# Optimization experiments

Hardware: AMD Instinct MI355X
Metric: run time of the kernel (lower is better)

The kernel has to match this reference:

```python
import jax, jax.numpy as jnp
import numpy as np

WS = 6          # window size
NUM_HEADS = 6
HEAD_DIM = 32   # dim=192 / 6 heads
SCALE = HEAD_DIM ** -0.5


def _rel_pos_index(ws):
    # Faithful to the torch buffer construction (torch.meshgrid default 'ij').
    coords = np.stack(np.meshgrid(np.arange(ws), np.arange(ws), np.arange(ws), indexing='ij'))  # [3,ws,ws,ws]
    flat = coords.reshape(3, -1)                       # [3, ws^3]
    rel = flat[:, :, None] - flat[:, None, :]          # [3, N, N]
    rel = rel.transpose(1, 2, 0).astype(np.int64)      # [N, N, 3]
    rel += ws - 1
    rel[..., 0] *= 3 * ws - 1
    rel[..., 1] *= 2 * ws - 1
    return rel.sum(-1)                                 # [N, N]

REL_INDEX = jnp.asarray(_rel_pos_index(WS))            # [216, 216] int


def setup_inputs() -> dict:
    key = jax.random.key(0)
    k1, k2, k3, k4 = jax.random.split(key, 4)
    B, N, C = 1024, WS ** 3, NUM_HEADS * HEAD_DIM
    return {
        "x": jax.random.normal(k1, (B, N, C), dtype=jnp.float32),
        "qkv_w": jax.random.normal(k2, (3 * C, C), dtype=jnp.float32) * 0.02,
        "proj_w": jax.random.normal(k3, (C, C), dtype=jnp.float32) * 0.02,
        "proj_b": jnp.zeros((C,), dtype=jnp.float32),
        "bias_table": jax.random.normal(k4, ((2 * WS - 1) ** 3, NUM_HEADS), dtype=jnp.float32) * 0.02,
    }


def reference(x, qkv_w, proj_w, proj_b, bias_table):
    B, N, C = x.shape
    H, D = NUM_HEADS, HEAD_DIM
    qkv = jnp.einsum('bnc,fc->bnf', x, qkv_w)              # [B,N,3C]
    qkv = qkv.reshape(B, N, 3, H, D).transpose(2, 0, 3, 1, 4)  # [3,B,H,N,D]
    q, k, v = qkv[0], qkv[1], qkv[2]
    attn = jnp.einsum('bhnd,bhmd->bhnm', q * SCALE, k)     # [B,H,N,N]
    bias = bias_table[REL_INDEX]                           # [N,N,H]
    attn = attn + bias.transpose(2, 0, 1)[None]            # add [1,H,N,N]
    attn = jax.nn.softmax(attn, axis=-1)
    out = jnp.einsum('bhnm,bhmd->bhnd', attn, v)           # [B,H,N,D]
    out = out.transpose(0, 2, 1, 3).reshape(B, N, C)
    return jnp.einsum('bnc,oc->bno', out, proj_w) + proj_b
```

## Files before the change

### kernel.cpp

```cpp
#include <hip/hip_runtime.h>
#include <cstdint>
#include <cstddef>


typedef __attribute__((ext_vector_type(8))) short short8;
typedef __attribute__((ext_vector_type(4))) float f32x4;
typedef unsigned short u16;
typedef unsigned int   u32;

#define SCALE_F 0.17677669529663687f

#define QS_OFF   0
#define KS_OFF   17920
#define VT_OFF   35840
#define ATTN_LDS 50688

#define PROJ_LDS 76800

__device__ __forceinline__ u16 f2bf(float f) {
  union { float f; u32 u; } v; v.f = f;
  return (u16)((v.u + 0x7fffu + ((v.u >> 16) & 1u)) >> 16);
}

__device__ __forceinline__ f32x4 mfma16(short8 a, short8 b, f32x4 c) {
  return __builtin_amdgcn_mfma_f32_16x16x32_bf16(a, b, c, 0, 0, 0);
}

__global__ void prep_kernel(const float* __restrict__ x,
                            const float* __restrict__ qkv_w,
                            const float* __restrict__ proj_w,
                            const float* __restrict__ bias_table,
                            u16* __restrict__ wb,
                            u16* __restrict__ pwb,
                            u16* __restrict__ biasp,
                            float* outbuf) {
  const int tid = blockIdx.x * blockDim.x + threadIdx.x;
  const int stride = gridDim.x * blockDim.x;
  const float4* x4 = (const float4*)x;
  for (int i = tid; i < 1024 * 10368; i += stride) {
    const int b = i / 10368, r = i % 10368;
    const float4 v = x4[i];
    union { u16 s[4]; unsigned long long u; } pk;
    pk.s[0] = f2bf(v.x); pk.s[1] = f2bf(v.y);
    pk.s[2] = f2bf(v.z); pk.s[3] = f2bf(v.w);
    *(unsigned long long*)((u16*)(outbuf + (size_t)b * 41472) + 41472 + r * 4) = pk.u;
  }
  for (int i = tid; i < 576 * 192; i += stride) wb[i] = f2bf(qkv_w[i]);
  for (int i = tid; i < 192 * 192; i += stride) pwb[i] = f2bf(proj_w[i]);
  for (int i = tid; i < 6 * 7 * 224 * 16 * 2; i += stride) {
    const int t = i & 1;
    int j = i >> 1;
    const int l = j & 15;  j >>= 4;
    const int n = j % 224; j /= 224;
    const int c = j % 7;
    const int h = j / 7;
    const int m = c * 32 + t * 16 + l;
    u16 val;
    if (n >= 216)      val = 0;
    else if (m >= 216) val = 0xFF80;
    else {
      const int di = n / 36 - m / 36;
      const int dj = (n / 6) % 6 - (m / 6) % 6;
      const int dk = n % 6 - m % 6;
      const int idx = (di + 5) * 17 + (dj + 5) * 11 + (dk + 5);
      val = f2bf(bias_table[idx * 6 + h]);
    }
    biasp[i] = val;
  }
}

__global__ __launch_bounds__(896, 7)
void attn_kernel(const u16* __restrict__ wb, const u16* __restrict__ biasp,
                 float* outbuf) {
  extern __shared__ char smem[];
  u16* qs  = (u16*)(smem + QS_OFF);
  u16* ks  = (u16*)(smem + KS_OFF);
  u16* vT  = (u16*)(smem + VT_OFF);

  const int b = blockIdx.x;
  const int tid = threadIdx.x;
  const int wave = tid >> 6;
  const int lane = tid & 63;
  const int quad = lane >> 4;
  const int lcol = lane & 15;

  const u16* xb    = (const u16*)(outbuf + (size_t)b * 41472) + 41472;
  u16*       attnb = (u16*)(outbuf + (size_t)b * 41472);

  for (int i = tid; i < 8 * 40; i += 896) { qs[216 * 40 + i] = 0; ks[216 * 40 + i] = 0; }
  for (int i = tid; i < 32 * 8; i += 896) {
    const int d = i >> 3, jj = i & 7;
    vT[d * 232 + 192 + 20 + (jj & 3) + ((jj >> 2) << 3)] = 0;
  }
  __syncthreads();

  for (int h = 0; h < 6; ++h) {
    {
      const int u = wave;
      f32x4 acc[6] = {};
      const int ar0 = u * 16 + lcol;
      const int ar  = ar0 < 216 ? ar0 : 215;
#pragma unroll
      for (int kk = 0; kk < 6; ++kk) {
        const short8 a = *(const short8*)(xb + ar * 192 + kk * 32 + quad * 8);
#pragma unroll
        for (int j = 0; j < 6; ++j) {
          const int fbase = (j >> 1) * 192 + h * 32 + (j & 1) * 16;
          const short8 bf = *(const short8*)(wb + (fbase + lcol) * 192 + kk * 32 + quad * 8);
          acc[j] = mfma16(a, bf, acc[j]);
        }
      }
      const int nb = u * 16 + quad * 4;
#pragma unroll
      for (int r = 0; r < 4; ++r) {
        const int n = nb + r;
        if (n < 216) {
          *(u32*)(qs + n * 40 + 2 * lcol) =
              (u32)f2bf(acc[0][r]) | ((u32)f2bf(acc[1][r]) << 16);
          *(u32*)(ks + n * 40 + 2 * lcol) =
              (u32)f2bf(acc[2][r]) | ((u32)f2bf(acc[3][r]) << 16);
          const int pm = (n & ~31) | (((n >> 2) & 3) << 3) | (((n >> 4) & 1) << 2) | (n & 3);
          vT[lcol * 232 + pm]        = f2bf(acc[4][r]);
          vT[(16 + lcol) * 232 + pm] = f2bf(acc[5][r]);
        }
      }
    }
    __syncthreads();

    {
      const int s = wave;
      const short8 qa = *(const short8*)(qs + (s * 16 + lcol) * 40 + quad * 8);
      f32x4 o0 = {}, o1 = {};
      float rsum = 0.0f;
#pragma unroll
      for (int c = 0; c < 7; ++c) {
        const short8 kb0 = *(const short8*)(ks + (c * 32 + lcol) * 40 + quad * 8);
        const short8 kb1 = *(const short8*)(ks + (c * 32 + 16 + lcol) * 40 + quad * 8);
        const f32x4 z = {};
        const f32x4 s0 = mfma16(kb0, qa, z);
        const f32x4 s1 = mfma16(kb1, qa, z);
        const uint4 bq = *(const uint4*)(biasp
            + ((size_t)((h * 7 + c) * 224 + s * 16 + lcol)) * 32 + quad * 8);
        const u32* bw = (const u32*)&bq;
        float p0[4], p1[4];
#pragma unroll
        for (int r = 0; r < 4; ++r) {
          union { u32 u; float f; } b0, b1;
          b0.u = bw[r] << 16;
          b1.u = bw[r] & 0xFFFF0000u;
          p0[r] = __expf(__builtin_fmaf(s0[r], SCALE_F, b0.f));
          p1[r] = __expf(__builtin_fmaf(s1[r], SCALE_F, b1.f));
          rsum += p0[r] + p1[r];
        }
        union { u32 w[4]; short8 v; } pk;
        pk.w[0] = (u32)f2bf(p0[0]) | ((u32)f2bf(p0[1]) << 16);
        pk.w[1] = (u32)f2bf(p0[2]) | ((u32)f2bf(p0[3]) << 16);
        pk.w[2] = (u32)f2bf(p1[0]) | ((u32)f2bf(p1[1]) << 16);
        pk.w[3] = (u32)f2bf(p1[2]) | ((u32)f2bf(p1[3]) << 16);
        const short8 vb0 = *(const short8*)(vT + lcol * 232 + c * 32 + quad * 8);
        const short8 vb1 = *(const short8*)(vT + (16 + lcol) * 232 + c * 32 + quad * 8);
        o0 = mfma16(pk.v, vb0, o0);
        o1 = mfma16(pk.v, vb1, o1);
      }
      rsum += __shfl_xor(rsum, 16);
      rsum += __shfl_xor(rsum, 32);
      const float inv = 1.0f / rsum;
#pragma unroll
      for (int r = 0; r < 4; ++r) {
        const float invr = __shfl(inv, quad * 4 + r, 16);
        const int n = s * 16 + quad * 4 + r;
        if (n < 216) {
          attnb[n * 192 + h * 32 + lcol]      = f2bf(o0[r] * invr);
          attnb[n * 192 + h * 32 + 16 + lcol] = f2bf(o1[r] * invr);
        }
      }
    }
    __syncthreads();
  }
}

__global__ __launch_bounds__(896, 7)
void proj_kernel(const u16* __restrict__ pwb, const float* __restrict__ proj_b,
                 float* outbuf) {
  extern __shared__ char smem[];
  u16* pws = (u16*)smem;
  const int b = blockIdx.x, tid = threadIdx.x;
  const int wave = tid >> 6, lane = tid & 63, quad = lane >> 4, lcol = lane & 15;
  float* myout = outbuf + (size_t)b * 41472;
  const u16* attnb = (const u16*)myout;

  for (int i = tid; i < 192 * 24; i += 896) {
    const int row = i / 24, c8 = i % 24;
    *(short8*)(pws + row * 200 + c8 * 8) = *(const short8*)(pwb + row * 192 + c8 * 8);
  }

  short8 a[6] = {};
  {
    const int arow = wave * 16 + lcol;
    if (arow < 216) {
#pragma unroll
      for (int kk = 0; kk < 6; ++kk)
        a[kk] = *(const short8*)(attnb + arow * 192 + kk * 32 + quad * 8);
    }
  }
  __syncthreads();

  for (int nt = 0; nt < 12; ++nt) {
    f32x4 acc = {};
#pragma unroll
    for (int kk = 0; kk < 6; ++kk) {
      const short8 bf = *(const short8*)(pws + (nt * 16 + lcol) * 200 + kk * 32 + quad * 8);
      acc = mfma16(a[kk], bf, acc);
    }
    const float pbv = proj_b[nt * 16 + lcol];
    const int nb = wave * 16 + quad * 4;
#pragma unroll
    for (int r = 0; r < 4; ++r) {
      const int n = nb + r;
      if (n < 216) myout[n * 192 + nt * 16 + lcol] = acc[r] + pbv;
    }
  }
}

extern "C" void kernel_launch(void* const* d_in, const int* in_sizes, int n_in,
                              void* d_out, int out_size, void* d_ws, size_t ws_size,
                              hipStream_t stream) {
  (void)in_sizes; (void)n_in; (void)out_size; (void)ws_size;
  const float* x          = (const float*)d_in[0];
  const float* qkv_w      = (const float*)d_in[1];
  const float* proj_w     = (const float*)d_in[2];
  const float* proj_b     = (const float*)d_in[3];
  const float* bias_table = (const float*)d_in[4];
  float* out = (float*)d_out;

  u16* wb    = (u16*)d_ws;
  u16* pwb   = (u16*)((char*)d_ws + 221184);
  u16* biasp = (u16*)((char*)d_ws + 294912);

  (void)hipFuncSetAttribute((const void*)attn_kernel,
                            hipFuncAttributeMaxDynamicSharedMemorySize, ATTN_LDS);
  (void)hipFuncSetAttribute((const void*)proj_kernel,
                            hipFuncAttributeMaxDynamicSharedMemorySize, PROJ_LDS);

  prep_kernel<<<dim3(1024), dim3(256), 0, stream>>>(x, qkv_w, proj_w, bias_table,
                                                    wb, pwb, biasp, out);
  attn_kernel<<<dim3(1024), dim3(896), ATTN_LDS, stream>>>(wb, biasp, out);
  proj_kernel<<<dim3(1024), dim3(896), PROJ_LDS, stream>>>(pwb, proj_b, out);
}
```

Before: 876.9 us.

## Double-buffer K/V and overlap next-head QKV projection with attention

Computes the next head's QKV projection inside the current head's attention loop, writing K and V into alternate LDS buffers. This halves the number of block barriers and interleaves MFMA work from both stages. The attention output is stored per head in contiguous layout, and the projection kernel's reads are adjusted to match. LDS use grows and blocks go to 1024 threads with two idle waves, which may reduce occupancy.

```diff
diff --git a/kernel.cpp b/kernel.cpp
--- a/kernel.cpp
+++ b/kernel.cpp
@@ -11,9 +11,11 @@
 #define SCALE_F 0.17677669529663687f
 
 #define QS_OFF   0
-#define KS_OFF   17920
-#define VT_OFF   35840
-#define ATTN_LDS 50688
+#define KS0_OFF  17280
+#define KS1_OFF  34560
+#define VT0_OFF  51840
+#define VT1_OFF  66688
+#define ATTN_LDS 81536
 
 #define PROJ_LDS 76800
 
@@ -69,13 +71,105 @@
   }
 }
 
-__global__ __launch_bounds__(896, 7)
+template <bool DOP1>
+__device__ __forceinline__ void head_step(
+    int h, const u16* __restrict__ xb, const u16* __restrict__ wb,
+    const u16* __restrict__ biasp, u16* __restrict__ attnb,
+    u16* qs, const u16* ksc, const u16* vtc, u16* ksn, u16* vtn,
+    int wave, int quad, int lcol) {
+  const int s = wave;
+  const int qr0 = s * 16 + lcol;
+  const int qr  = qr0 < 216 ? qr0 : 215;
+  const short8 qa = *(const short8*)(qs + qr * 40 + quad * 8);
+
+  f32x4 acc[6] = {};
+  const int ar = qr;
+
+  f32x4 o0 = {}, o1 = {};
+  float rsum = 0.0f;
+
+#pragma unroll
+  for (int c = 0; c < 7; ++c) {
+    const short8 kb0 = *(const short8*)(ksc + (c * 32 + lcol) * 40 + quad * 8);
+    const int kr1 = c * 32 + 16 + lcol;
+    const short8 kb1 = *(const short8*)(ksc + (kr1 < 216 ? kr1 : 215) * 40 + quad * 8);
+    const f32x4 z = {};
+    const f32x4 s0 = mfma16(kb0, qa, z);
+    const f32x4 s1 = mfma16(kb1, qa, z);
+    const uint4 bq = *(const uint4*)(biasp
+        + ((size_t)((h * 7 + c) * 224 + s * 16 + lcol)) * 32 + quad * 8);
+    const u32* bw = (const u32*)&bq;
+    float p0[4], p1[4];
+#pragma unroll
+    for (int r = 0; r < 4; ++r) {
+      union { u32 u; float f; } b0, b1;
+      b0.u = bw[r] << 16;
+      b1.u = bw[r] & 0xFFFF0000u;
+      p0[r] = __expf(__builtin_fmaf(s0[r], SCALE_F, b0.f));
+      p1[r] = __expf(__builtin_fmaf(s1[r], SCALE_F, b1.f));
+      rsum += p0[r] + p1[r];
+    }
+    union { u32 w[4]; short8 v; } pk;
+    pk.w[0] = (u32)f2bf(p0[0]) | ((u32)f2bf(p0[1]) << 16);
+    pk.w[1] = (u32)f2bf(p0[2]) | ((u32)f2bf(p0[3]) << 16);
+    pk.w[2] = (u32)f2bf(p1[0]) | ((u32)f2bf(p1[1]) << 16);
+    pk.w[3] = (u32)f2bf(p1[2]) | ((u32)f2bf(p1[3]) << 16);
+    const short8 vb0 = *(const short8*)(vtc + lcol * 232 + c * 32 + quad * 8);
+    const short8 vb1 = *(const short8*)(vtc + (16 + lcol) * 232 + c * 32 + quad * 8);
+    o0 = mfma16(pk.v, vb0, o0);
+    o1 = mfma16(pk.v, vb1, o1);
+
+    if (DOP1 && c < 6) {
+      const short8 a = *(const short8*)(xb + ar * 192 + c * 32 + quad * 8);
+#pragma unroll
+      for (int j = 0; j < 6; ++j) {
+        const int fbase = (j >> 1) * 192 + (h + 1) * 32 + (j & 1) * 16;
+        const short8 bf = *(const short8*)(wb + (fbase + lcol) * 192 + c * 32 + quad * 8);
+        acc[j] = mfma16(a, bf, acc[j]);
+      }
+    }
+  }
+
+  rsum += __shfl_xor(rsum, 16);
+  rsum += __shfl_xor(rsum, 32);
+  const float inv = 1.0f / rsum;
+#pragma unroll
+  for (int r = 0; r < 4; ++r) {
+    const float invr = __shfl(inv, quad * 4 + r, 16);
+    const int n = s * 16 + quad * 4 + r;
+    if (n < 216) {
+      attnb[(h * 216 + n) * 32 + lcol]      = f2bf(o0[r] * invr);
+      attnb[(h * 216 + n) * 32 + 16 + lcol] = f2bf(o1[r] * invr);
+    }
+  }
+
+  if (DOP1) {
+    const int nb = s * 16 + quad * 4;
+#pragma unroll
+    for (int r = 0; r < 4; ++r) {
+      const int n = nb + r;
+      if (n < 216) {
+        *(u32*)(qs + n * 40 + 2 * lcol) =
+            (u32)f2bf(acc[0][r]) | ((u32)f2bf(acc[1][r]) << 16);
+        *(u32*)(ksn + n * 40 + 2 * lcol) =
+            (u32)f2bf(acc[2][r]) | ((u32)f2bf(acc[3][r]) << 16);
+        const int pm = (n & ~31) | (((n >> 2) & 3) << 3) | (((n >> 4) & 1) << 2) | (n & 3);
+        vtn[lcol * 232 + pm]        = f2bf(acc[4][r]);
+        vtn[(16 + lcol) * 232 + pm] = f2bf(acc[5][r]);
+      }
+    }
+  }
+}
+
+__global__ __launch_bounds__(1024, 8)
 void attn_kernel(const u16* __restrict__ wb, const u16* __restrict__ biasp,
                  float* outbuf) {
   extern __shared__ char smem[];
   u16* qs  = (u16*)(smem + QS_OFF);
-  u16* ks  = (u16*)(smem + KS_OFF);
-  u16* vT  = (u16*)(smem + VT_OFF);
+  u16* ks0 = (u16*)(smem + KS0_OFF);
+  u16* ks1 = (u16*)(smem + KS1_OFF);
+  u16* vt0 = (u16*)(smem + VT0_OFF);
+  u16* vt1 = (u16*)(smem + VT1_OFF);
 
   const int b = blockIdx.x;
   const int tid = threadIdx.x;
@@ -83,103 +177,67 @@
   const int lane = tid & 63;
   const int quad = lane >> 4;
   const int lcol = lane & 15;
+  const bool active = wave < 14;
 
   const u16* xb    = (const u16*)(outbuf + (size_t)b * 41472) + 41472;
   u16*       attnb = (u16*)(outbuf + (size_t)b * 41472);
 
-  for (int i = tid; i < 8 * 40; i += 896) { qs[216 * 40 + i] = 0; ks[216 * 40 + i] = 0; }
-  for (int i = tid; i < 32 * 8; i += 896) {
-    const int d = i >> 3, jj = i & 7;
-    vT[d * 232 + 192 + 20 + (jj & 3) + ((jj >> 2) << 3)] = 0;
+  for (int i = tid; i < 512; i += 1024) {
+    const int bufi = i >> 8;
+    const int d  = (i >> 3) & 31;
+    const int jj = i & 7;
+    u16* vt = bufi ? vt1 : vt0;
+    vt[d * 232 + 192 + 20 + (jj & 3) + ((jj >> 2) << 3)] = 0;
+  }
+
+  if (active) {
+    f32x4 acc[6] = {};
+    const int ar0 = wave * 16 + lcol;
+    const int ar  = ar0 < 216 ? ar0 : 215;
+#pragma unroll
+    for (int kk = 0; kk < 6; ++kk) {
+      const short8 a = *(const short8*)(xb + ar * 192 + kk * 32 + quad * 8);
+#pragma unroll
+      for (int j = 0; j < 6; ++j) {
+        const int fbase = (j >> 1) * 192 + (j & 1) * 16;
+        const short8 bf = *(const short8*)(wb + (fbase + lcol) * 192 + kk * 32 + quad * 8);
+        acc[j] = mfma16(a, bf, acc[j]);
+      }
+    }
+    const int nb = wave * 16 + quad * 4;
+#pragma unroll
+    for (int r = 0; r < 4; ++r) {
+      const int n = nb + r;
+      if (n < 216) {
+        *(u32*)(qs + n * 40 + 2 * lcol) =
+            (u32)f2bf(acc[0][r]) | ((u32)f2bf(acc[1][r]) << 16);
+        *(u32*)(ks0 + n * 40 + 2 * lcol) =
+            (u32)f2bf(acc[2][r]) | ((u32)f2bf(acc[3][r]) << 16);
+        const int pm = (n & ~31) | (((n >> 2) & 3) << 3) | (((n >> 4) & 1) << 2) | (n & 3);
+        vt0[lcol * 232 + pm]        = f2bf(acc[4][r]);
+        vt0[(16 + lcol) * 232 + pm] = f2bf(acc[5][r]);
+      }
+    }
   }
   __syncthreads();
 
-  for (int h = 0; h < 6; ++h) {
-    {
-      const int u = wave;
-      f32x4 acc[6] = {};
-      const int ar0 = u * 16 + lcol;
-      const int ar  = ar0 < 216 ? ar0 : 215;
-#pragma unroll
-      for (int kk = 0; kk < 6; ++kk) {
-        const short8 a = *(const short8*)(xb + ar * 192 + kk * 32 + quad * 8);
-#pragma unroll
-        for (int j = 0; j < 6; ++j) {
-          const int fbase = (j >> 1) * 192 + h * 32 + (j & 1) * 16;
-          const short8 bf = *(const short8*)(wb + (fbase + lcol) * 192 + kk * 32 + quad * 8);
-          acc[j] = mfma16(a, bf, acc[j]);
-        }
-      }
-      const int nb = u * 16 + quad * 4;
-#pragma unroll
-      for (int r = 0; r < 4; ++r) {
-        const int n = nb + r;
-        if (n < 216) {
-          *(u32*)(qs + n * 40 + 2 * lcol) =
-              (u32)f2bf(acc[0][r]) | ((u32)f2bf(acc[1][r]) << 16);
-          *(u32*)(ks + n * 40 + 2 * lcol) =
-              (u32)f2bf(acc[2][r]) | ((u32)f2bf(acc[3][r]) << 16);
-          const int pm = (n & ~31) | (((n >> 2) & 3) << 3) | (((n >> 4) & 1) << 2) | (n & 3);
-          vT[lcol * 232 + pm]        = f2bf(acc[4][r]);
-          vT[(16 + lcol) * 232 + pm] = f2bf(acc[5][r]);
-        }
-      }
-    }
+  for (int h = 0; h < 5; ++h) {
+    const bool even = (h & 1) == 0;
+    const u16* ksc = even ? ks0 : ks1;
+    const u16* vtc = even ? vt0 : vt1;
+    u16* ksn = even ? ks1 : ks0;
+    u16* vtn = even ? vt1 : vt0;
+    if (active)
+      head_step<true>(h, xb, wb, biasp, attnb, qs, ksc, vtc, ksn, vtn,
+                      wave, quad, lcol);
     __syncthreads();
-
-    {
-      const int s = wave;
-      const short8 qa = *(const short8*)(qs + (s * 16 + lcol) * 40 + quad * 8);
-      f32x4 o0 = {}, o1 = {};
-      float rsum = 0.0f;
-#pragma unroll
-      for (int c = 0; c < 7; ++c) {
-        const short8 kb0 = *(const short8*)(ks + (c * 32 + lcol) * 40 + quad * 8);
-        const short8 kb1 = *(const short8*)(ks + (c * 32 + 16 + lcol) * 40 + quad * 8);
-        const f32x4 z = {};
-        const f32x4 s0 = mfma16(kb0, qa, z);
-        const f32x4 s1 = mfma16(kb1, qa, z);
-        const uint4 bq = *(const uint4*)(biasp
-            + ((size_t)((h * 7 + c) * 224 + s * 16 + lcol)) * 32 + quad * 8);
-        const u32* bw = (const u32*)&bq;
-        float p0[4], p1[4];
-#pragma unroll
-        for (int r = 0; r < 4; ++r) {
-          union { u32 u; float f; } b0, b1;
-          b0.u = bw[r] << 16;
-          b1.u = bw[r] & 0xFFFF0000u;
-          p0[r] = __expf(__builtin_fmaf(s0[r], SCALE_F, b0.f));
-          p1[r] = __expf(__builtin_fmaf(s1[r], SCALE_F, b1.f));
-          rsum += p0[r] + p1[r];
-        }
-        union { u32 w[4]; short8 v; } pk;
-        pk.w[0] = (u32)f2bf(p0[0]) | ((u32)f2bf(p0[1]) << 16);
-        pk.w[1] = (u32)f2bf(p0[2]) | ((u32)f2bf(p0[3]) << 16);
-        pk.w[2] = (u32)f2bf(p1[0]) | ((u32)f2bf(p1[1]) << 16);
-        pk.w[3] = (u32)f2bf(p1[2]) | ((u32)f2bf(p1[3]) << 16);
-        const short8 vb0 = *(const short8*)(vT + lcol * 232 + c * 32 + quad * 8);
-        const short8 vb1 = *(const short8*)(vT + (16 + lcol) * 232 + c * 32 + quad * 8);
-        o0 = mfma16(pk.v, vb0, o0);
-        o1 = mfma16(pk.v, vb1, o1);
-      }
-      rsum += __shfl_xor(rsum, 16);
-      rsum += __shfl_xor(rsum, 32);
-      const float inv = 1.0f / rsum;
-#pragma unroll
-      for (int r = 0; r < 4; ++r) {
-        const float invr = __shfl(inv, quad * 4 + r, 16);
-        const int n = s * 16 + quad * 4 + r;
-        if (n < 216) {
-          attnb[n * 192 + h * 32 + lcol]      = f2bf(o0[r] * invr);
-          attnb[n * 192 + h * 32 + 16 + lcol] = f2bf(o1[r] * invr);
-        }
-      }
-    }
-    __syncthreads();
-  }
-}
-
-__global__ __launch_bounds__(896, 7)
+  }
+  if (active)
+    head_step<false>(5, xb, wb, biasp, attnb, qs, ks1, vt1, ks0, vt0,
+                     wave, quad, lcol);
+}
+
+__global__ __launch_bounds__(1024, 8)
 void proj_kernel(const u16* __restrict__ pwb, const float* __restrict__ proj_b,
                  float* outbuf) {
   extern __shared__ char smem[];
@@ -189,35 +247,38 @@
   float* myout = outbuf + (size_t)b * 41472;
   const u16* attnb = (const u16*)myout;
 
-  for (int i = tid; i < 192 * 24; i += 896) {
+  for (int i = tid; i < 192 * 24; i += 1024) {
     const int row = i / 24, c8 = i % 24;
     *(short8*)(pws + row * 200 + c8 * 8) = *(const short8*)(pwb + row * 192 + c8 * 8);
   }
 
   short8 a[6] = {};
-  {
+  const bool active = wave < 14;
+  if (active) {
     const int arow = wave * 16 + lcol;
     if (arow < 216) {
 #pragma unroll
       for (int kk = 0; kk < 6; ++kk)
-        a[kk] = *(const short8*)(attnb + arow * 192 + kk * 32 + quad * 8);
+        a[kk] = *(const short8*)(attnb + (kk * 216 + arow) * 32 + quad * 8);
     }
   }
   __syncthreads();
 
-  for (int nt = 0; nt < 12; ++nt) {
-    f32x4 acc = {};
-#pragma unroll
-    for (int kk = 0; kk < 6; ++kk) {
-      const short8 bf = *(const short8*)(pws + (nt * 16 + lcol) * 200 + kk * 32 + quad * 8);
-      acc = mfma16(a[kk], bf, acc);
-    }
-    const float pbv = proj_b[nt * 16 + lcol];
-    const int nb = wave * 16 + quad * 4;
-#pragma unroll
-    for (int r = 0; r < 4; ++r) {
-      const int n = nb + r;
-      if (n < 216) myout[n * 192 + nt * 16 + lcol] = acc[r] + pbv;
+  if (active) {
+    for (int nt = 0; nt < 12; ++nt) {
+      f32x4 acc = {};
+#pragma unroll
+      for (int kk = 0; kk < 6; ++kk) {
+        const short8 bf = *(const short8*)(pws + (nt * 16 + lcol) * 200 + kk * 32 + quad * 8);
+        acc = mfma16(a[kk], bf, acc);
+      }
+      const float pbv = proj_b[nt * 16 + lcol];
+      const int nb = wave * 16 + quad * 4;
+#pragma unroll
+      for (int r = 0; r < 4; ++r) {
+        const int n = nb + r;
+        if (n < 216) myout[n * 192 + nt * 16 + lcol] = acc[r] + pbv;
+      }
     }
   }
 }
@@ -244,6 +305,6 @@
 
   prep_kernel<<<dim3(1024), dim3(256), 0, stream>>>(x, qkv_w, proj_w, bias_table,
                                                     wb, pwb, biasp, out);
-  attn_kernel<<<dim3(1024), dim3(896), ATTN_LDS, stream>>>(wb, biasp, out);
-  proj_kernel<<<dim3(1024), dim3(896), PROJ_LDS, stream>>>(pwb, proj_b, out);
-}
+  attn_kernel<<<dim3(1024), dim3(1024), ATTN_LDS, stream>>>(wb, biasp, out);
+  proj_kernel<<<dim3(1024), dim3(1024), PROJ_LDS, stream>>>(pwb, proj_b, out);
+}
```

Measured after the change: 1.189 ms. 35.5% more time.
